# Kernel optimization log

Measured on AMD Instinct MI355X. Metric: run time of the kernel, lower is better.

The kernel has to match this reference:

```python
import jax, jax.numpy as jnp
import numpy as np

B = 4096
NP = 196  # 14x14 patches


def setup_inputs() -> dict:
    key = jax.random.key(0)
    k1, k2, k3 = jax.random.split(key, 3)
    x = jax.random.uniform(k1, (B, 1, 28, 28), dtype=jnp.float32)
    params = jax.random.normal(k2, (8,), dtype=jnp.float32)      # [rz0, ry0, rz1, ry1, ...]
    W = jax.random.normal(k3, (10, 784), dtype=jnp.float32) * 0.03
    b = jnp.zeros((10,), dtype=jnp.float32)
    return {"x": x, "params": params, "W": W, "b": b}


def reference(x, params, W, b):
    bsz = x.shape[0]
    # Extract 2x2 patches: per-patch qubit order [x[r,c], x[r,c+1], x[r+1,c], x[r+1,c+1]]
    d = x.reshape(bsz, 14, 2, 14, 2).transpose(0, 1, 3, 2, 4).reshape(bsz, NP, 4)
    alpha = params[0::2]  # rz angles, per wire [4]
    beta = params[1::2]   # ry angles, per wire [4]
    # Per-wire single-qubit chain on |0>: Ry(beta) Rz(alpha) Ry(d) Ry(d) |0>
    # Ry(2d)|0> = [cos d, sin d]; then Rz phases; then Ry(beta) rotation.
    cb = jnp.cos(0.5 * beta)
    sb = jnp.sin(0.5 * beta)
    pm = jnp.exp(-0.5j * alpha)  # e^{-i a/2}
    pp = jnp.exp(0.5j * alpha)   # e^{+i a/2}
    a = pm * jnp.cos(d)          # [B,P,4] complex64
    c = pp * jnp.sin(d)
    u = jnp.stack([cb * a - sb * c, sb * a + cb * c], axis=-1)  # [B,P,4,2]
    # Product state over 4 wires -> [B,P,2,2,2,2]
    st = jnp.einsum('bpi,bpj,bpk,bpl->bpijkl',
                    u[:, :, 0], u[:, :, 1], u[:, :, 2], u[:, :, 3])
    # CNOT(0,1): flip target axis (j) where control axis (i) == 1
    st = jnp.concatenate([st[:, :, 0:1], st[:, :, 1:2, ::-1]], axis=2)
    # CNOT(2,3): flip target axis (l) where control axis (k) == 1
    st = jnp.concatenate([st[:, :, :, :, 0:1, :], st[:, :, :, :, 1:2, ::-1]], axis=4)
    probs = (st * jnp.conj(st)).real  # [B,P,2,2,2,2]
    z = jnp.array([1.0, -1.0], dtype=jnp.float32)
    e0 = jnp.einsum('bpijkl,i->bp', probs, z)
    e1 = jnp.einsum('bpijkl,j->bp', probs, z)
    e2 = jnp.einsum('bpijkl,k->bp', probs, z)
    e3 = jnp.einsum('bpijkl,l->bp', probs, z)
    feats = jnp.stack([e0, e1, e2, e3], axis=-1).reshape(bsz, NP * 4)  # patch-major, matches torch.cat
    logits = feats @ W.T + b
    return jax.nn.log_softmax(logits, axis=-1)
```

## Files before the change

kernel.cpp:

```cpp
#include <hip/hip_runtime.h>
#include <math.h>


__global__ __launch_bounds__(256) void quanv_kernel(
    const float* __restrict__ x,
    const float* __restrict__ params,
    const float* __restrict__ W,
    const float* __restrict__ bias,
    float* __restrict__ out)
{
    const int b = blockIdx.x;
    const int t = threadIdx.x;

    __shared__ float s_img[784];
    __shared__ float s_A[4], s_B[4];
    __shared__ float s_red[4][10];

    if (t < 4) {
        float al = params[2 * t];
        float be = params[2 * t + 1];
        s_A[t] = cosf(be);
        s_B[t] = sinf(be) * cosf(al);
    }

    const float* xb = x + (size_t)b * 784;
    for (int i = t; i < 784; i += 256) s_img[i] = xb[i];
    __syncthreads();

    float logit[10];
#pragma unroll
    for (int c = 0; c < 10; c++) logit[c] = 0.0f;

    if (t < 196) {
        const int i = t / 14;
        const int j = t - 14 * i;
        const int base = (2 * i) * 28 + 2 * j;
        const float d0 = s_img[base];
        const float d1 = s_img[base + 1];
        const float d2 = s_img[base + 28];
        const float d3 = s_img[base + 29];

        float s, c;
        sincosf(2.0f * d0, &s, &c); const float E0 = s_A[0] * c - s_B[0] * s;
        sincosf(2.0f * d1, &s, &c); const float E1 = s_A[1] * c - s_B[1] * s;
        sincosf(2.0f * d2, &s, &c); const float E2 = s_A[2] * c - s_B[2] * s;
        sincosf(2.0f * d3, &s, &c); const float E3 = s_A[3] * c - s_B[3] * s;

        const float f0 = E0;
        const float f1 = E0 * E1;
        const float f2 = E2;
        const float f3 = E2 * E3;

        const float* Wp = W + 4 * t;
#pragma unroll
        for (int c2 = 0; c2 < 10; c2++) {
            const float* wr = Wp + c2 * 784;
            logit[c2] = f0 * wr[0] + f1 * wr[1] + f2 * wr[2] + f3 * wr[3];
        }
    }

#pragma unroll
    for (int c = 0; c < 10; c++) {
        float v = logit[c];
#pragma unroll
        for (int off = 32; off > 0; off >>= 1) v += __shfl_down(v, off, 64);
        logit[c] = v;
    }
    const int wave = t >> 6;
    const int lane = t & 63;
    if (lane == 0) {
#pragma unroll
        for (int c = 0; c < 10; c++) s_red[wave][c] = logit[c];
    }
    __syncthreads();

    if (t == 0) {
        float lg[10];
        float mx = -1e30f;
#pragma unroll
        for (int c = 0; c < 10; c++) {
            lg[c] = s_red[0][c] + s_red[1][c] + s_red[2][c] + s_red[3][c] + bias[c];
            mx = fmaxf(mx, lg[c]);
        }
        float sum = 0.0f;
#pragma unroll
        for (int c = 0; c < 10; c++) sum += expf(lg[c] - mx);
        const float lse = mx + logf(sum);
        float* ob = out + (size_t)b * 10;
#pragma unroll
        for (int c = 0; c < 10; c++) ob[c] = lg[c] - lse;
    }
}

extern "C" void kernel_launch(void* const* d_in, const int* in_sizes, int n_in,
                              void* d_out, int out_size, void* d_ws, size_t ws_size,
                              hipStream_t stream) {
    const float* x      = (const float*)d_in[0];
    const float* params = (const float*)d_in[1];
    const float* W      = (const float*)d_in[2];
    const float* bias   = (const float*)d_in[3];
    float* out          = (float*)d_out;

    quanv_kernel<<<4096, 256, 0, stream>>>(x, params, W, bias, out);
}
```

Measured before the change: 81.01 us.

## Map one wavefront per image and drop cross-wave shared reduction

Each 256-thread block now handles four images, one per wavefront, so every lane loops over patches and the logits reduce with wave shuffles alone, with no shared-memory reduction or second barrier. The image load is vectorised with float4 and the W rows are read as float4. Fast intrinsics (__sinf, __cosf, __expf, __logf) replace the precise math calls. This cuts launched blocks and barriers and uses all lanes, in exchange for lower accuracy from the fast math and each lane doing several patches in sequence.

```diff
diff --git a/kernel.cpp b/kernel.cpp
--- a/kernel.cpp
+++ b/kernel.cpp
@@ -9,83 +9,82 @@
     const float* __restrict__ bias,
     float* __restrict__ out)
 {
-    const int b = blockIdx.x;
     const int t = threadIdx.x;
+    const int wave = t >> 6;
+    const int lane = t & 63;
+    const int b = blockIdx.x * 4 + wave;
 
-    __shared__ float s_img[784];
-    __shared__ float s_A[4], s_B[4];
-    __shared__ float s_red[4][10];
+    __shared__ float s_img[4][784];
 
-    if (t < 4) {
-        float al = params[2 * t];
-        float be = params[2 * t + 1];
-        s_A[t] = cosf(be);
-        s_B[t] = sinf(be) * cosf(al);
+    {
+        const float4* src = (const float4*)(x + (size_t)blockIdx.x * 4 * 784);
+        float4* dst = (float4*)(&s_img[0][0]);
+        for (int i = t; i < 784; i += 256) dst[i] = src[i];
     }
 
-    const float* xb = x + (size_t)b * 784;
-    for (int i = t; i < 784; i += 256) s_img[i] = xb[i];
+    float A[4], Bc[4];
+#pragma unroll
+    for (int k = 0; k < 4; k++) {
+        const float al = params[2 * k];
+        const float be = params[2 * k + 1];
+        A[k]  = __cosf(be);
+        Bc[k] = __sinf(be) * __cosf(al);
+    }
+
     __syncthreads();
 
-    float logit[10];
+    float lg[10];
 #pragma unroll
-    for (int c = 0; c < 10; c++) logit[c] = 0.0f;
+    for (int c = 0; c < 10; c++) lg[c] = 0.0f;
 
-    if (t < 196) {
-        const int i = t / 14;
-        const int j = t - 14 * i;
-        const int base = (2 * i) * 28 + 2 * j;
-        const float d0 = s_img[base];
-        const float d1 = s_img[base + 1];
-        const float d2 = s_img[base + 28];
-        const float d3 = s_img[base + 29];
+    const float* img = s_img[wave];
+    const float4* W4 = (const float4*)W;
 
-        float s, c;
-        sincosf(2.0f * d0, &s, &c); const float E0 = s_A[0] * c - s_B[0] * s;
-        sincosf(2.0f * d1, &s, &c); const float E1 = s_A[1] * c - s_B[1] * s;
-        sincosf(2.0f * d2, &s, &c); const float E2 = s_A[2] * c - s_B[2] * s;
-        sincosf(2.0f * d3, &s, &c); const float E3 = s_A[3] * c - s_B[3] * s;
+    for (int p = lane; p < 196; p += 64) {
+        const int i = p / 14;
+        const int j = p - 14 * i;
+        const int base = i * 56 + 2 * j;
+        const float d0 = img[base];
+        const float d1 = img[base + 1];
+        const float d2 = img[base + 28];
+        const float d3 = img[base + 29];
+
+        const float E0 = A[0] * __cosf(2.0f * d0) - Bc[0] * __sinf(2.0f * d0);
+        const float E1 = A[1] * __cosf(2.0f * d1) - Bc[1] * __sinf(2.0f * d1);
+        const float E2 = A[2] * __cosf(2.0f * d2) - Bc[2] * __sinf(2.0f * d2);
+        const float E3 = A[3] * __cosf(2.0f * d3) - Bc[3] * __sinf(2.0f * d3);
 
         const float f0 = E0;
         const float f1 = E0 * E1;
         const float f2 = E2;
         const float f3 = E2 * E3;
 
-        const float* Wp = W + 4 * t;
 #pragma unroll
-        for (int c2 = 0; c2 < 10; c2++) {
-            const float* wr = Wp + c2 * 784;
-            logit[c2] = f0 * wr[0] + f1 * wr[1] + f2 * wr[2] + f3 * wr[3];
+        for (int c = 0; c < 10; c++) {
+            const float4 w = W4[c * 196 + p];
+            lg[c] += f0 * w.x + f1 * w.y + f2 * w.z + f3 * w.w;
         }
     }
 
 #pragma unroll
     for (int c = 0; c < 10; c++) {
-        float v = logit[c];
+        float v = lg[c];
 #pragma unroll
         for (int off = 32; off > 0; off >>= 1) v += __shfl_down(v, off, 64);
-        logit[c] = v;
+        lg[c] = v;
     }
-    const int wave = t >> 6;
-    const int lane = t & 63;
+
     if (lane == 0) {
-#pragma unroll
-        for (int c = 0; c < 10; c++) s_red[wave][c] = logit[c];
-    }
-    __syncthreads();
-
-    if (t == 0) {
-        float lg[10];
         float mx = -1e30f;
 #pragma unroll
         for (int c = 0; c < 10; c++) {
-            lg[c] = s_red[0][c] + s_red[1][c] + s_red[2][c] + s_red[3][c] + bias[c];
+            lg[c] += bias[c];
             mx = fmaxf(mx, lg[c]);
         }
         float sum = 0.0f;
 #pragma unroll
-        for (int c = 0; c < 10; c++) sum += expf(lg[c] - mx);
-        const float lse = mx + logf(sum);
+        for (int c = 0; c < 10; c++) sum += __expf(lg[c] - mx);
+        const float lse = mx + __logf(sum);
         float* ob = out + (size_t)b * 10;
 #pragma unroll
         for (int c = 0; c < 10; c++) ob[c] = lg[c] - lse;
@@ -101,5 +100,5 @@
     const float* bias   = (const float*)d_in[3];
     float* out          = (float*)d_out;
 
-    quanv_kernel<<<4096, 256, 0, stream>>>(x, params, W, bias, out);
+    quanv_kernel<<<1024, 256, 0, stream>>>(x, params, W, bias, out);
 }
```

Measured after the change: 71.22 us. 1.14x faster.
